# Kernel optimization log

Measured on AMD Instinct MI355X. Metric: run time of the kernel, lower is better.

Reference implementation:

```python
import jax, jax.numpy as jnp
import numpy as np

N, M, D, E, NLAYER = 200000, 100000, 64, 1000000, 3
EPS = 0.1
TLEN = (24, 7)


def l2norm(x):
    # F.normalize(dim=-1) with eps=1e-12 clamp on the norm
    n = jnp.linalg.norm(x, axis=-1, keepdims=True)
    return x / jnp.maximum(n, 1e-12)


def setup_inputs() -> dict:
    key = jax.random.key(0)
    ks = jax.random.split(key, 8)
    u_id = jax.random.randint(ks[0], (E,), 0, N)
    i_id = jax.random.randint(ks[1], (E,), 0, M)
    T = jnp.stack([
        jax.random.randint(ks[2], (E,), 0, TLEN[0]),
        jax.random.randint(ks[3], (E,), 0, TLEN[1]),
    ], axis=1)
    # xavier-uniform-ish init for embedding tables
    lim_u = np.sqrt(6.0 / (N + D)).astype(np.float32)
    lim_i = np.sqrt(6.0 / (M + D)).astype(np.float32)
    user_emb = jax.random.uniform(ks[4], (N, D), minval=-lim_u, maxval=lim_u)
    item_emb = jax.random.uniform(ks[5], (M, D), minval=-lim_i, maxval=lim_i)
    # xavier-normal time tables, each [tlen_i, D//tdim]
    W0 = jax.random.normal(ks[6], (TLEN[0], D // 2)) * np.sqrt(2.0 / (TLEN[0] + D // 2))
    W1 = jax.random.normal(ks[7], (TLEN[1], D // 2)) * np.sqrt(2.0 / (TLEN[1] + D // 2))
    beta = jnp.float32(0.3)
    return {"u_id": u_id, "i_id": i_id, "T": T, "beta": beta,
            "user_emb": user_emb, "item_emb": item_emb, "W0": W0, "W1": W1}


def _forward(u_id, i_id, T, beta, user_emb, item_emb, W0, W1):
    # TimeEncoder: one_hot(t) @ W == W[t]; concat over time dims -> [E, D]
    t_emb = jnp.concatenate([W0[T[:, 0]], W1[T[:, 1]]], axis=-1)
    u_t = l2norm(user_emb[u_id] + t_emb)
    i_t = l2norm(item_emb[i_id] + t_emb)
    s = ((u_t * i_t).sum(axis=-1) + 1.0) * 0.5      # cosine sim mapped to [0,1]
    s = jnp.where(s < beta, 0.0, s)                  # threshold

    # coalesced sparse COO mm: duplicates are summed by segment_sum anyway
    def spmm_u(X):  # A_r @ X : [n, d]
        return jax.ops.segment_sum(s[:, None] * X[i_id], u_id, num_segments=N)

    def spmm_i(X):  # A_r.T @ X : [m, d]
        return jax.ops.segment_sum(s[:, None] * X[u_id], i_id, num_segments=M)

    # pass 1: clean propagation
    u_embs, i_embs = [user_emb], [item_emb]
    for _ in range(NLAYER):
        u_embs.append(spmm_u(i_embs[-1]))
        i_embs.append(spmm_i(u_embs[-2]))
    u_fwd = jnp.mean(jnp.stack(u_embs[1:], 0), 0)
    i_fwd = jnp.mean(jnp.stack(i_embs[1:], 0), 0)

    # passes 2 & 3: perturbed propagation with randperm-row noise
    def perturbed_pass(base_key):
        u_embs, i_embs = [user_emb], [item_emb]
        for l in range(NLAYER):
            ku, ki = jax.random.split(jax.random.fold_in(base_key, l))
            u_emb = spmm_u(i_embs[-1])
            i_emb = spmm_i(u_embs[-1])
            u_emb = u_emb + l2norm(u_emb[jax.random.permutation(ku, N)]) * EPS
            i_emb = i_emb + l2norm(i_emb[jax.random.permutation(ki, M)]) * EPS
            u_embs.append(u_emb)
            i_embs.append(i_emb)
        return (jnp.mean(jnp.stack(u_embs[1:], 0), 0),
                jnp.mean(jnp.stack(i_embs[1:], 0), 0))

    u_p1, i_p1 = perturbed_pass(jax.random.key(1))
    u_p2, i_p2 = perturbed_pass(jax.random.key(2))
    return u_fwd, i_fwd, u_p1, i_p1, u_p2, i_p2


def reference(u_id, i_id, T, beta, user_emb, item_emb, W0, W1):
    return _forward(u_id, i_id, T, beta, user_emb, item_emb, W0, W1)
```

## Files before the change

### kernel.cpp

```cpp
#include <hip/hip_runtime.h>
#include <stdint.h>

#define NU 200000
#define NI 100000
#define DD 64
#define NE 1000000
#define EPSV 0.1f
#define NBUCK 65536
#define NSORT 12
#define PAIR (NU + NI)
#define TOTSORT (6 * PAIR)
#define NBALL (NSORT * NBUCK)
#define SCAN_TPB 256
#define SCAN_ELEMS 1024
#define CEILDIV(a,b) (((a)+(b)-1)/(b))

__host__ __device__ inline void tf2x32(uint32_t k0, uint32_t k1,
                                       uint32_t x0, uint32_t x1,
                                       uint32_t &o0, uint32_t &o1) {
  uint32_t ks0 = k0, ks1 = k1, ks2 = k0 ^ k1 ^ 0x1BD11BDAu;
  x0 += ks0; x1 += ks1;
#define TF_RND(r) { x0 += x1; x1 = (x1 << (r)) | (x1 >> (32 - (r))); x1 ^= x0; }
  TF_RND(13) TF_RND(15) TF_RND(26) TF_RND(6)   x0 += ks1; x1 += ks2 + 1u;
  TF_RND(17) TF_RND(29) TF_RND(16) TF_RND(24)  x0 += ks2; x1 += ks0 + 2u;
  TF_RND(13) TF_RND(15) TF_RND(26) TF_RND(6)   x0 += ks0; x1 += ks1 + 3u;
  TF_RND(17) TF_RND(29) TF_RND(16) TF_RND(24)  x0 += ks1; x1 += ks2 + 4u;
  TF_RND(13) TF_RND(15) TF_RND(26) TF_RND(6)   x0 += ks2; x1 += ks0 + 5u;
#undef TF_RND
  o0 = x0; o1 = x1;
}

struct K2 { uint32_t a, b; };
static inline K2 h_tf(K2 k, uint32_t x0, uint32_t x1) {
  K2 r; tf2x32(k.a, k.b, x0, x1, r.a, r.b); return r;
}

struct SortKeys { uint32_t a[NSORT]; uint32_t b[NSORT]; };

__device__ inline void regionOf(int gid, int &r, int &local) {
  int pairIdx = gid / PAIR;
  int rem = gid - pairIdx * PAIR;
  if (rem < NU) { r = pairIdx * 2;     local = rem; }
  else          { r = pairIdx * 2 + 1; local = rem - NU; }
}

__global__ void k_edge(const int* __restrict__ u_id, const int* __restrict__ i_id,
                       const int* __restrict__ T, const float* __restrict__ betap,
                       const float* __restrict__ UE, const float* __restrict__ IE,
                       const float* __restrict__ W0, const float* __restrict__ W1,
                       float* __restrict__ s)
{
  int g = blockIdx.x * blockDim.x + threadIdx.x;
  int e = g >> 4, lane = g & 15;
  if (e >= NE) return;
  int u = u_id[e], it = i_id[e];
  float4 a = ((const float4*)UE)[u * 16 + lane];
  float4 b = ((const float4*)IE)[it * 16 + lane];
  float4 t;
  if (lane < 8) t = ((const float4*)W0)[T[2 * e] * 8 + lane];
  else          t = ((const float4*)W1)[T[2 * e + 1] * 8 + (lane - 8)];
  float ux = a.x + t.x, uy = a.y + t.y, uz = a.z + t.z, uw = a.w + t.w;
  float ix = b.x + t.x, iy = b.y + t.y, iz = b.z + t.z, iw = b.w + t.w;
  float uu = ux * ux + uy * uy + uz * uz + uw * uw;
  float ii = ix * ix + iy * iy + iz * iz + iw * iw;
  float ui = ux * ix + uy * iy + uz * iz + uw * iw;
#pragma unroll
  for (int m = 1; m < 16; m <<= 1) {
    uu += __shfl_xor(uu, m);
    ii += __shfl_xor(ii, m);
    ui += __shfl_xor(ui, m);
  }
  if (lane == 0) {
    float c = ui / (fmaxf(sqrtf(uu), 1e-12f) * fmaxf(sqrtf(ii), 1e-12f));
    float sv = (c + 1.0f) * 0.5f;
    s[e] = (sv < betap[0]) ? 0.0f : sv;
  }
}

__global__ void k_scan1(const int* __restrict__ in, int n, int* __restrict__ partials)
{
  __shared__ int sdata[SCAN_TPB];
  int base = blockIdx.x * SCAN_ELEMS;
  int sum = 0;
  for (int j = threadIdx.x; j < SCAN_ELEMS; j += SCAN_TPB) {
    int idx = base + j;
    if (idx < n) sum += in[idx];
  }
  sdata[threadIdx.x] = sum;
  __syncthreads();
  for (int off = SCAN_TPB / 2; off > 0; off >>= 1) {
    if (threadIdx.x < off) sdata[threadIdx.x] += sdata[threadIdx.x + off];
    __syncthreads();
  }
  if (threadIdx.x == 0) partials[blockIdx.x] = sdata[0];
}

__global__ void k_scan2(int* __restrict__ partials, int nb, int* __restrict__ endPtr)
{
  __shared__ int part[1024];
  int tid = threadIdx.x;
  part[tid] = (tid < nb) ? partials[tid] : 0;
  __syncthreads();
  for (int off = 1; off < 1024; off <<= 1) {
    int t = (tid >= off) ? part[tid - off] : 0;
    __syncthreads();
    part[tid] += t;
    __syncthreads();
  }
  if (tid < nb) partials[tid] = tid ? part[tid - 1] : 0;
  if (tid == 1023 && endPtr) *endPtr = part[1023];
}

__global__ void k_scan3(const int* __restrict__ in, int n,
                        const int* __restrict__ partials,
                        int* __restrict__ offs, int* __restrict__ cursor)
{
  __shared__ int sdata[SCAN_TPB];
  int base = blockIdx.x * SCAN_ELEMS + threadIdx.x * 4;
  int v[4];
#pragma unroll
  for (int q = 0; q < 4; ++q) v[q] = (base + q < n) ? in[base + q] : 0;
  int tsum = v[0] + v[1] + v[2] + v[3];
  sdata[threadIdx.x] = tsum;
  __syncthreads();
  for (int off = 1; off < SCAN_TPB; off <<= 1) {
    int t = (threadIdx.x >= off) ? sdata[threadIdx.x - off] : 0;
    __syncthreads();
    sdata[threadIdx.x] += t;
    __syncthreads();
  }
  int excl = partials[blockIdx.x] + (threadIdx.x ? sdata[threadIdx.x - 1] : 0);
#pragma unroll
  for (int q = 0; q < 4; ++q) {
    if (base + q < n) {
      offs[base + q] = excl;
      if (cursor) cursor[base + q] = excl;
      excl += v[q];
    }
  }
}

static void scan_ex(hipStream_t st, const int* in, int n, int* offs, int* cursor,
                    int* partials, int* endPtr)
{
  int nb = CEILDIV(n, SCAN_ELEMS);
  k_scan1<<<nb, SCAN_TPB, 0, st>>>(in, n, partials);
  k_scan2<<<1, 1024, 0, st>>>(partials, nb, endPtr);
  k_scan3<<<nb, SCAN_TPB, 0, st>>>(in, n, partials, offs, cursor);
}

__global__ void k_count(const int* __restrict__ u_id, const int* __restrict__ i_id,
                        int* __restrict__ cnt_u, int* __restrict__ cnt_i)
{
  int e = blockIdx.x * blockDim.x + threadIdx.x;
  if (e < NE) {
    atomicAdd(&cnt_u[u_id[e]], 1);
    atomicAdd(&cnt_i[i_id[e]], 1);
  }
}

__global__ void k_scatter_csr(const int* __restrict__ u_id, const int* __restrict__ i_id,
                              const float* __restrict__ s,
                              int* __restrict__ cur_u, int* __restrict__ cur_i,
                              int* __restrict__ col_u, float* __restrict__ w_u,
                              int* __restrict__ col_i, float* __restrict__ w_i)
{
  int e = blockIdx.x * blockDim.x + threadIdx.x;
  if (e < NE) {
    float w = s[e];
    int pu = atomicAdd(&cur_u[u_id[e]], 1);
    col_u[pu] = i_id[e]; w_u[pu] = w;
    int pi = atomicAdd(&cur_i[i_id[e]], 1);
    col_i[pi] = u_id[e]; w_i[pi] = w;
  }
}

__global__ void k_spmm(const int* __restrict__ ptr, const int* __restrict__ col,
                       const float* __restrict__ w, const float* __restrict__ X,
                       float* __restrict__ Y, float* __restrict__ acc,
                       int nrows, int first, float scale)
{
  int g = blockIdx.x * blockDim.x + threadIdx.x;
  int r = g >> 4, lane = g & 15;
  if (r >= nrows) return;
  int b = ptr[r], e2 = ptr[r + 1];
  float4 a = make_float4(0.f, 0.f, 0.f, 0.f);
  for (int k = b; k < e2; ++k) {
    float wk = w[k];
    int c = col[k];
    float4 x = ((const float4*)X)[c * 16 + lane];
    a.x += wk * x.x; a.y += wk * x.y; a.z += wk * x.z; a.w += wk * x.w;
  }
  ((float4*)Y)[r * 16 + lane] = a;
  if (acc) {
    float4 v;
    if (first) v = a;
    else {
      v = ((const float4*)acc)[r * 16 + lane];
      v.x += a.x; v.y += a.y; v.z += a.z; v.w += a.w;
    }
    v.x *= scale; v.y *= scale; v.z *= scale; v.w *= scale;
    ((float4*)acc)[r * 16 + lane] = v;
  }
}

__global__ void k_noise(const float* __restrict__ S, const int* __restrict__ perm,
                        float* __restrict__ O, float* __restrict__ acc,
                        int nrows, int first, float scale)
{
  int g = blockIdx.x * blockDim.x + threadIdx.x;
  int r = g >> 4, lane = g & 15;
  if (r >= nrows) return;
  int pr = perm[r];
  float4 z = ((const float4*)S)[pr * 16 + lane];
  float ss = z.x * z.x + z.y * z.y + z.z * z.z + z.w * z.w;
#pragma unroll
  for (int m = 1; m < 16; m <<= 1) ss += __shfl_xor(ss, m);
  float coef = EPSV / fmaxf(sqrtf(ss), 1e-12f);
  float4 v = ((const float4*)S)[r * 16 + lane];
  v.x += coef * z.x; v.y += coef * z.y; v.z += coef * z.z; v.w += coef * z.w;
  ((float4*)O)[r * 16 + lane] = v;
  float4 a;
  if (first) a = v;
  else {
    a = ((const float4*)acc)[r * 16 + lane];
    a.x += v.x; a.y += v.y; a.z += v.z; a.w += v.w;
  }
  a.x *= scale; a.y *= scale; a.z *= scale; a.w *= scale;
  ((float4*)acc)[r * 16 + lane] = a;
}

__global__ void k_genkeys_all(SortKeys sk, uint32_t* __restrict__ keys)
{
  int gid = blockIdx.x * blockDim.x + threadIdx.x;
  if (gid >= TOTSORT) return;
  int r, local; regionOf(gid, r, local);
  uint32_t o0, o1;
  tf2x32(sk.a[r], sk.b[r], 0u, (uint32_t)local, o0, o1);
  keys[gid] = o0 ^ o1;
}

__global__ void k_hist_all(const uint32_t* __restrict__ keys, int* __restrict__ hist)
{
  int gid = blockIdx.x * blockDim.x + threadIdx.x;
  if (gid >= TOTSORT) return;
  int r, local; regionOf(gid, r, local);
  atomicAdd(&hist[r * NBUCK + (keys[gid] >> 16)], 1);
}

__global__ void k_scatter_all(const uint32_t* __restrict__ keys,
                              const int* __restrict__ valsIn,
                              int* __restrict__ cursor,
                              uint32_t* __restrict__ keyO, int* __restrict__ valO,
                              int* __restrict__ posO)
{
  int gid = blockIdx.x * blockDim.x + threadIdx.x;
  if (gid >= TOTSORT) return;
  int r, local; regionOf(gid, r, local);
  uint32_t k = keys[gid];
  int p = atomicAdd(&cursor[r * NBUCK + (k >> 16)], 1);
  keyO[p] = k;
  valO[p] = valsIn ? valsIn[gid] : local;
  posO[p] = local;
}

__global__ void k_fixup(const int* __restrict__ offs, uint32_t* __restrict__ keyO,
                        int* __restrict__ valO, int* __restrict__ posO)
{
  int b = blockIdx.x * blockDim.x + threadIdx.x;
  if (b >= NBALL) return;
  int s0 = offs[b], e0 = offs[b + 1];
  for (int i = s0 + 1; i < e0; ++i) {
    uint32_t k = keyO[i]; int v = valO[i], p = posO[i];
    int j = i - 1;
    while (j >= s0 && (keyO[j] > k || (keyO[j] == k && posO[j] > p))) {
      keyO[j + 1] = keyO[j]; valO[j + 1] = valO[j]; posO[j + 1] = posO[j];
      --j;
    }
    keyO[j + 1] = k; valO[j + 1] = v; posO[j + 1] = p;
  }
}

extern "C" void kernel_launch(void* const* d_in, const int* in_sizes, int n_in,
                              void* d_out, int out_size, void* d_ws, size_t ws_size,
                              hipStream_t stream)
{
  const int*   u_id = (const int*)d_in[0];
  const int*   i_id = (const int*)d_in[1];
  const int*   T    = (const int*)d_in[2];
  const float* beta = (const float*)d_in[3];
  const float* UE   = (const float*)d_in[4];
  const float* IE   = (const float*)d_in[5];
  const float* W0   = (const float*)d_in[6];
  const float* W1   = (const float*)d_in[7];
  (void)in_sizes; (void)n_in; (void)out_size; (void)ws_size;

  float* out   = (float*)d_out;
  float* o_ufw = out;
  float* o_ifw = o_ufw + (size_t)NU * DD;
  float* o_up1 = o_ifw + (size_t)NI * DD;
  float* o_ip1 = o_up1 + (size_t)NU * DD;
  float* o_up2 = o_ip1 + (size_t)NI * DD;
  float* o_ip2 = o_up2 + (size_t)NU * DD;

  char* wp = (char*)d_ws;
  auto carve = [&](size_t bytes) -> char* {
    char* r = wp; wp += (bytes + 255) & ~(size_t)255; return r;
  };
  int*      ptr_u    = (int*)  carve(4ull * (NU + 1));
  int*      cnt_u    = (int*)  carve(4ull * NU);
  int*      cur_u    = (int*)  carve(4ull * NU);
  int*      ptr_i    = (int*)  carve(4ull * (NI + 1));
  int*      cnt_i    = (int*)  carve(4ull * NI);
  int*      cur_i    = (int*)  carve(4ull * NI);
  int*      col_u    = (int*)  carve(4ull * NE);
  float*    w_u      = (float*)carve(4ull * NE);
  int*      col_i    = (int*)  carve(4ull * NE);
  float*    w_i      = (float*)carve(4ull * NE);
  int*      perms    = (int*)  carve(4ull * TOTSORT);
  int*      partials = (int*)  carve(4ull * 1025);
  char*     uni      =         carve(4ull * 2 * (size_t)(NU + NI) * DD);

  float* U1 = (float*)uni;
  float* U2 = U1 + (size_t)NU * DD;
  float* I1 = U2 + (size_t)NU * DD;
  float* I2 = I1 + (size_t)NI * DD;
  float* s = (float*)uni;
  uint32_t* keysA = (uint32_t*)uni;
  uint32_t* keyB  = keysA + TOTSORT;
  int*      posB  = (int*)(keyB + TOTSORT);
  int*      val0  = posB + TOTSORT;
  int*      hist  = val0 + TOTSORT;
  int*      offs  = hist + NBALL;
  int*      curs  = offs + NBALL + 1;

  k_edge<<<CEILDIV(NE * 16, 256), 256, 0, stream>>>(u_id, i_id, T, beta, UE, IE, W0, W1, s);

  hipMemsetAsync(cnt_u, 0, 4 * NU, stream);
  hipMemsetAsync(cnt_i, 0, 4 * NI, stream);
  k_count<<<CEILDIV(NE, 256), 256, 0, stream>>>(u_id, i_id, cnt_u, cnt_i);
  scan_ex(stream, cnt_u, NU, ptr_u, cur_u, partials, &ptr_u[NU]);
  scan_ex(stream, cnt_i, NI, ptr_i, cur_i, partials, &ptr_i[NI]);
  k_scatter_csr<<<CEILDIV(NE, 256), 256, 0, stream>>>(u_id, i_id, s, cur_u, cur_i,
                                                      col_u, w_u, col_i, w_i);

  SortKeys sk0, sk1;
  for (int p = 0; p < 2; ++p) {
    K2 base = {0u, (uint32_t)(p + 1)};
    for (int l = 0; l < 3; ++l) {
      K2 kl = h_tf(base, 0u, (uint32_t)l);
      K2 kk[2] = { h_tf(kl, 0u, 0u), h_tf(kl, 0u, 1u) };
      for (int q = 0; q < 2; ++q) {
        int r = (p * 3 + l) * 2 + q;
        K2 kperm = kk[q];
        K2 knext = h_tf(kperm, 0u, 0u);
        K2 sub0  = h_tf(kperm, 0u, 1u);
        K2 sub1  = h_tf(knext, 0u, 1u);
        sk0.a[r] = sub0.a; sk0.b[r] = sub0.b;
        sk1.a[r] = sub1.a; sk1.b[r] = sub1.b;
      }
    }
  }
  const int GS = CEILDIV(TOTSORT, 256), GF = CEILDIV(NBALL, 256);
  k_genkeys_all<<<GS, 256, 0, stream>>>(sk0, keysA);
  hipMemsetAsync(hist, 0, 4ull * NBALL, stream);
  k_hist_all<<<GS, 256, 0, stream>>>(keysA, hist);
  scan_ex(stream, hist, NBALL, offs, curs, partials, &offs[NBALL]);
  k_scatter_all<<<GS, 256, 0, stream>>>(keysA, (const int*)nullptr, curs, keyB, val0, posB);
  k_fixup<<<GF, 256, 0, stream>>>(offs, keyB, val0, posB);
  k_genkeys_all<<<GS, 256, 0, stream>>>(sk1, keysA);
  hipMemsetAsync(hist, 0, 4ull * NBALL, stream);
  k_hist_all<<<GS, 256, 0, stream>>>(keysA, hist);
  scan_ex(stream, hist, NBALL, offs, curs, partials, &offs[NBALL]);
  k_scatter_all<<<GS, 256, 0, stream>>>(keysA, val0, curs, keyB, perms, posB);
  k_fixup<<<GF, 256, 0, stream>>>(offs, keyB, perms, posB);

  const int GU = CEILDIV(NU * 16, 256), GI = CEILDIV(NI * 16, 256);
  const float THIRD = 1.0f / 3.0f;

  k_spmm<<<GU, 256, 0, stream>>>(ptr_u, col_u, w_u, IE, U1, o_ufw, NU, 1, 1.0f);
  k_spmm<<<GI, 256, 0, stream>>>(ptr_i, col_i, w_i, UE, I1, o_ifw, NI, 1, 1.0f);
  k_spmm<<<GU, 256, 0, stream>>>(ptr_u, col_u, w_u, I1, U2, o_ufw, NU, 0, 1.0f);
  k_spmm<<<GI, 256, 0, stream>>>(ptr_i, col_i, w_i, U1, I2, o_ifw, NI, 0, 1.0f);
  k_spmm<<<GU, 256, 0, stream>>>(ptr_u, col_u, w_u, I2, U1, o_ufw, NU, 0, THIRD);
  k_spmm<<<GI, 256, 0, stream>>>(ptr_i, col_i, w_i, U2, I1, o_ifw, NI, 0, THIRD);

  for (int p = 0; p < 2; ++p) {
    float* accU = (p == 0) ? o_up1 : o_up2;
    float* accI = (p == 0) ? o_ip1 : o_ip2;
    const float* uP = UE;
    const float* iP = IE;
    for (int l = 0; l < 3; ++l) {
      int* permU = perms + (size_t)(p * 3 + l) * PAIR;
      int* permI = permU + NU;
      int first = (l == 0), isLast = (l == 2);
      float sc = isLast ? THIRD : 1.0f;
      k_spmm<<<GU, 256, 0, stream>>>(ptr_u, col_u, w_u, iP, U1, (float*)nullptr, NU, 0, 1.0f);
      k_spmm<<<GI, 256, 0, stream>>>(ptr_i, col_i, w_i, uP, I1, (float*)nullptr, NI, 0, 1.0f);
      k_noise<<<GU, 256, 0, stream>>>(U1, permU, U2, accU, NU, first, sc);
      k_noise<<<GI, 256, 0, stream>>>(I1, permI, I2, accI, NI, first, sc);
      uP = U2; iP = I2;
    }
  }
}
```

Baseline: 2.301 ms.

## Fuse edge scoring with CSR scatter, merge user/item SpMM, reuse first-layer propagation

Edge similarity is now computed and scattered straight into CSR, storing column index and weight together as one uint2. This removes the separate scatter kernel and the round trip through the s array. User and item SpMM and noise kernels now run as single launches over both row sets. When workspace allows a third buffer, the first-layer propagation of the clean pass is reused by both perturbed passes, since all three start from the same input embeddings. Unneeded intermediate writes are skipped on last layers, at the cost of more workspace and a branchy combined kernel.

New measurement: 1.957 ms. 15.0% less time.

```diff
diff --git a/kernel.cpp b/kernel.cpp
--- a/kernel.cpp
+++ b/kernel.cpp
@@ -44,11 +44,12 @@
   else          { r = pairIdx * 2 + 1; local = rem - NU; }
 }
 
-__global__ void k_edge(const int* __restrict__ u_id, const int* __restrict__ i_id,
-                       const int* __restrict__ T, const float* __restrict__ betap,
-                       const float* __restrict__ UE, const float* __restrict__ IE,
-                       const float* __restrict__ W0, const float* __restrict__ W1,
-                       float* __restrict__ s)
+__global__ void k_edgesc(const int* __restrict__ u_id, const int* __restrict__ i_id,
+                         const int* __restrict__ T, const float* __restrict__ betap,
+                         const float* __restrict__ UE, const float* __restrict__ IE,
+                         const float* __restrict__ W0, const float* __restrict__ W1,
+                         int* __restrict__ cur_u, int* __restrict__ cur_i,
+                         uint2* __restrict__ colw_u, uint2* __restrict__ colw_i)
 {
   int g = blockIdx.x * blockDim.x + threadIdx.x;
   int e = g >> 4, lane = g & 15;
@@ -73,7 +74,12 @@
   if (lane == 0) {
     float c = ui / (fmaxf(sqrtf(uu), 1e-12f) * fmaxf(sqrtf(ii), 1e-12f));
     float sv = (c + 1.0f) * 0.5f;
-    s[e] = (sv < betap[0]) ? 0.0f : sv;
+    float w = (sv < betap[0]) ? 0.0f : sv;
+    uint32_t wb = __float_as_uint(w);
+    int pu = atomicAdd(&cur_u[u], 1);
+    colw_u[pu] = make_uint2((uint32_t)it, wb);
+    int pi = atomicAdd(&cur_i[it], 1);
+    colw_i[pi] = make_uint2((uint32_t)u, wb);
   }
 }
 
@@ -159,39 +165,28 @@
   }
 }
 
-__global__ void k_scatter_csr(const int* __restrict__ u_id, const int* __restrict__ i_id,
-                              const float* __restrict__ s,
-                              int* __restrict__ cur_u, int* __restrict__ cur_i,
-                              int* __restrict__ col_u, float* __restrict__ w_u,
-                              int* __restrict__ col_i, float* __restrict__ w_i)
-{
-  int e = blockIdx.x * blockDim.x + threadIdx.x;
-  if (e < NE) {
-    float w = s[e];
-    int pu = atomicAdd(&cur_u[u_id[e]], 1);
-    col_u[pu] = i_id[e]; w_u[pu] = w;
-    int pi = atomicAdd(&cur_i[i_id[e]], 1);
-    col_i[pi] = u_id[e]; w_i[pi] = w;
-  }
-}
-
-__global__ void k_spmm(const int* __restrict__ ptr, const int* __restrict__ col,
-                       const float* __restrict__ w, const float* __restrict__ X,
-                       float* __restrict__ Y, float* __restrict__ acc,
-                       int nrows, int first, float scale)
+__global__ void k_spmm2(const int* __restrict__ ptr_u, const uint2* __restrict__ colw_u,
+                        const float* __restrict__ Xi_in,
+                        const int* __restrict__ ptr_i, const uint2* __restrict__ colw_i,
+                        const float* __restrict__ Xu_in,
+                        float* __restrict__ Y, float* __restrict__ acc,
+                        int first, float scale, int writeY)
 {
   int g = blockIdx.x * blockDim.x + threadIdx.x;
   int r = g >> 4, lane = g & 15;
-  if (r >= nrows) return;
-  int b = ptr[r], e2 = ptr[r + 1];
+  if (r >= PAIR) return;
+  const int* ptr; const uint2* colw; const float4* X; int rr;
+  if (r < NU) { ptr = ptr_u; colw = colw_u; X = (const float4*)Xi_in; rr = r; }
+  else        { ptr = ptr_i; colw = colw_i; X = (const float4*)Xu_in; rr = r - NU; }
+  int b = ptr[rr], e2 = ptr[rr + 1];
   float4 a = make_float4(0.f, 0.f, 0.f, 0.f);
   for (int k = b; k < e2; ++k) {
-    float wk = w[k];
-    int c = col[k];
-    float4 x = ((const float4*)X)[c * 16 + lane];
+    uint2 cw = colw[k];
+    float wk = __uint_as_float(cw.y);
+    float4 x = X[(size_t)cw.x * 16 + lane];
     a.x += wk * x.x; a.y += wk * x.y; a.z += wk * x.z; a.w += wk * x.w;
   }
-  ((float4*)Y)[r * 16 + lane] = a;
+  if (writeY) ((float4*)Y)[r * 16 + lane] = a;
   if (acc) {
     float4 v;
     if (first) v = a;
@@ -204,22 +199,22 @@
   }
 }
 
-__global__ void k_noise(const float* __restrict__ S, const int* __restrict__ perm,
-                        float* __restrict__ O, float* __restrict__ acc,
-                        int nrows, int first, float scale)
+__global__ void k_noise2(const float* __restrict__ S, const int* __restrict__ perm,
+                         float* __restrict__ O, float* __restrict__ acc,
+                         int first, float scale, int writeO)
 {
   int g = blockIdx.x * blockDim.x + threadIdx.x;
   int r = g >> 4, lane = g & 15;
-  if (r >= nrows) return;
-  int pr = perm[r];
-  float4 z = ((const float4*)S)[pr * 16 + lane];
+  if (r >= PAIR) return;
+  int pr = (r < NU) ? perm[r] : NU + perm[r];
+  float4 z = ((const float4*)S)[(size_t)pr * 16 + lane];
   float ss = z.x * z.x + z.y * z.y + z.z * z.z + z.w * z.w;
 #pragma unroll
   for (int m = 1; m < 16; m <<= 1) ss += __shfl_xor(ss, m);
   float coef = EPSV / fmaxf(sqrtf(ss), 1e-12f);
-  float4 v = ((const float4*)S)[r * 16 + lane];
+  float4 v = ((const float4*)S)[(size_t)r * 16 + lane];
   v.x += coef * z.x; v.y += coef * z.y; v.z += coef * z.z; v.w += coef * z.w;
-  ((float4*)O)[r * 16 + lane] = v;
+  if (writeO) ((float4*)O)[r * 16 + lane] = v;
   float4 a;
   if (first) a = v;
   else {
@@ -293,39 +288,37 @@
   const float* IE   = (const float*)d_in[5];
   const float* W0   = (const float*)d_in[6];
   const float* W1   = (const float*)d_in[7];
-  (void)in_sizes; (void)n_in; (void)out_size; (void)ws_size;
-
-  float* out   = (float*)d_out;
-  float* o_ufw = out;
-  float* o_ifw = o_ufw + (size_t)NU * DD;
-  float* o_up1 = o_ifw + (size_t)NI * DD;
-  float* o_ip1 = o_up1 + (size_t)NU * DD;
-  float* o_up2 = o_ip1 + (size_t)NI * DD;
-  float* o_ip2 = o_up2 + (size_t)NU * DD;
+  (void)in_sizes; (void)n_in; (void)out_size;
+
+  float* out    = (float*)d_out;
+  float* accCln = out;
+  float* accP0  = out + (size_t)PAIR * DD;
+  float* accP1  = out + 2ull * PAIR * DD;
 
   char* wp = (char*)d_ws;
   auto carve = [&](size_t bytes) -> char* {
     char* r = wp; wp += (bytes + 255) & ~(size_t)255; return r;
   };
-  int*      ptr_u    = (int*)  carve(4ull * (NU + 1));
-  int*      cnt_u    = (int*)  carve(4ull * NU);
-  int*      cur_u    = (int*)  carve(4ull * NU);
-  int*      ptr_i    = (int*)  carve(4ull * (NI + 1));
-  int*      cnt_i    = (int*)  carve(4ull * NI);
-  int*      cur_i    = (int*)  carve(4ull * NI);
-  int*      col_u    = (int*)  carve(4ull * NE);
-  float*    w_u      = (float*)carve(4ull * NE);
-  int*      col_i    = (int*)  carve(4ull * NE);
-  float*    w_i      = (float*)carve(4ull * NE);
-  int*      perms    = (int*)  carve(4ull * TOTSORT);
-  int*      partials = (int*)  carve(4ull * 1025);
-  char*     uni      =         carve(4ull * 2 * (size_t)(NU + NI) * DD);
-
-  float* U1 = (float*)uni;
-  float* U2 = U1 + (size_t)NU * DD;
-  float* I1 = U2 + (size_t)NU * DD;
-  float* I2 = I1 + (size_t)NI * DD;
-  float* s = (float*)uni;
+  int*   ptr_u    = (int*)  carve(4ull * (NU + 1));
+  int*   cnt_u    = (int*)  carve(4ull * NU);
+  int*   cur_u    = (int*)  carve(4ull * NU);
+  int*   ptr_i    = (int*)  carve(4ull * (NI + 1));
+  int*   cnt_i    = (int*)  carve(4ull * NI);
+  int*   cur_i    = (int*)  carve(4ull * NI);
+  uint2* colw_u   = (uint2*)carve(8ull * NE);
+  uint2* colw_i   = (uint2*)carve(8ull * NE);
+  int*   perms    = (int*)  carve(4ull * TOTSORT);
+  int*   partials = (int*)  carve(4ull * 1025);
+
+  const size_t PB = (size_t)PAIR * DD * 4;
+  size_t used = (size_t)(wp - (char*)d_ws);
+  bool share = ws_size >= used + 3 * PB;
+  char* uni = carve(share ? 3 * PB : 2 * PB);
+
+  float* P0 = (float*)uni;
+  float* P1 = P0 + (size_t)PAIR * DD;
+  float* P2 = share ? P1 + (size_t)PAIR * DD : nullptr;
+
   uint32_t* keysA = (uint32_t*)uni;
   uint32_t* keyB  = keysA + TOTSORT;
   int*      posB  = (int*)(keyB + TOTSORT);
@@ -334,15 +327,14 @@
   int*      offs  = hist + NBALL;
   int*      curs  = offs + NBALL + 1;
 
-  k_edge<<<CEILDIV(NE * 16, 256), 256, 0, stream>>>(u_id, i_id, T, beta, UE, IE, W0, W1, s);
-
   hipMemsetAsync(cnt_u, 0, 4 * NU, stream);
   hipMemsetAsync(cnt_i, 0, 4 * NI, stream);
   k_count<<<CEILDIV(NE, 256), 256, 0, stream>>>(u_id, i_id, cnt_u, cnt_i);
   scan_ex(stream, cnt_u, NU, ptr_u, cur_u, partials, &ptr_u[NU]);
   scan_ex(stream, cnt_i, NI, ptr_i, cur_i, partials, &ptr_i[NI]);
-  k_scatter_csr<<<CEILDIV(NE, 256), 256, 0, stream>>>(u_id, i_id, s, cur_u, cur_i,
-                                                      col_u, w_u, col_i, w_i);
+  k_edgesc<<<CEILDIV(NE * 16, 256), 256, 0, stream>>>(u_id, i_id, T, beta, UE, IE,
+                                                      W0, W1, cur_u, cur_i,
+                                                      colw_u, colw_i);
 
   SortKeys sk0, sk1;
   for (int p = 0; p < 2; ++p) {
@@ -375,31 +367,43 @@
   k_scatter_all<<<GS, 256, 0, stream>>>(keysA, val0, curs, keyB, perms, posB);
   k_fixup<<<GF, 256, 0, stream>>>(offs, keyB, perms, posB);
 
-  const int GU = CEILDIV(NU * 16, 256), GI = CEILDIV(NI * 16, 256);
+  const int GP = CEILDIV(PAIR * 16, 256);
   const float THIRD = 1.0f / 3.0f;
-
-  k_spmm<<<GU, 256, 0, stream>>>(ptr_u, col_u, w_u, IE, U1, o_ufw, NU, 1, 1.0f);
-  k_spmm<<<GI, 256, 0, stream>>>(ptr_i, col_i, w_i, UE, I1, o_ifw, NI, 1, 1.0f);
-  k_spmm<<<GU, 256, 0, stream>>>(ptr_u, col_u, w_u, I1, U2, o_ufw, NU, 0, 1.0f);
-  k_spmm<<<GI, 256, 0, stream>>>(ptr_i, col_i, w_i, U1, I2, o_ifw, NI, 0, 1.0f);
-  k_spmm<<<GU, 256, 0, stream>>>(ptr_u, col_u, w_u, I2, U1, o_ufw, NU, 0, THIRD);
-  k_spmm<<<GI, 256, 0, stream>>>(ptr_i, col_i, w_i, U2, I1, o_ifw, NI, 0, THIRD);
-
-  for (int p = 0; p < 2; ++p) {
-    float* accU = (p == 0) ? o_up1 : o_up2;
-    float* accI = (p == 0) ? o_ip1 : o_ip2;
-    const float* uP = UE;
-    const float* iP = IE;
-    for (int l = 0; l < 3; ++l) {
-      int* permU = perms + (size_t)(p * 3 + l) * PAIR;
-      int* permI = permU + NU;
-      int first = (l == 0), isLast = (l == 2);
-      float sc = isLast ? THIRD : 1.0f;
-      k_spmm<<<GU, 256, 0, stream>>>(ptr_u, col_u, w_u, iP, U1, (float*)nullptr, NU, 0, 1.0f);
-      k_spmm<<<GI, 256, 0, stream>>>(ptr_i, col_i, w_i, uP, I1, (float*)nullptr, NI, 0, 1.0f);
-      k_noise<<<GU, 256, 0, stream>>>(U1, permU, U2, accU, NU, first, sc);
-      k_noise<<<GI, 256, 0, stream>>>(I1, permI, I2, accI, NI, first, sc);
-      uP = U2; iP = I2;
-    }
-  }
-}
+  auto SPMM = [&](const float* Xi_in, const float* Xu_in, float* Y, float* acc,
+                  int first, float scale, int writeY) {
+    k_spmm2<<<GP, 256, 0, stream>>>(ptr_u, colw_u, Xi_in, ptr_i, colw_i, Xu_in,
+                                    Y, acc, first, scale, writeY);
+  };
+  auto NOISE = [&](const float* S, int pass, int layer, float* O, float* acc,
+                   int first, float scale, int writeO) {
+    k_noise2<<<GP, 256, 0, stream>>>(S, perms + (size_t)(pass * 3 + layer) * PAIR,
+                                     O, acc, first, scale, writeO);
+  };
+
+  if (share) {
+    SPMM(IE, UE, P0, accCln, 1, 1.0f, 1);
+    SPMM(P0 + (size_t)NU * DD, P0, P1, accCln, 0, 1.0f, 1);
+    SPMM(P1 + (size_t)NU * DD, P1, nullptr, accCln, 0, THIRD, 0);
+    for (int p = 0; p < 2; ++p) {
+      float* acc = p ? accP1 : accP0;
+      NOISE(P0, p, 0, P1, acc, 1, 1.0f, 1);
+      SPMM(P1 + (size_t)NU * DD, P1, P2, nullptr, 0, 1.0f, 1);
+      NOISE(P2, p, 1, P1, acc, 0, 1.0f, 1);
+      SPMM(P1 + (size_t)NU * DD, P1, P2, nullptr, 0, 1.0f, 1);
+      NOISE(P2, p, 2, nullptr, acc, 0, THIRD, 0);
+    }
+  } else {
+    SPMM(IE, UE, P0, accCln, 1, 1.0f, 1);
+    SPMM(P0 + (size_t)NU * DD, P0, P1, accCln, 0, 1.0f, 1);
+    SPMM(P1 + (size_t)NU * DD, P1, nullptr, accCln, 0, THIRD, 0);
+    for (int p = 0; p < 2; ++p) {
+      float* acc = p ? accP1 : accP0;
+      SPMM(IE, UE, P0, nullptr, 0, 1.0f, 1);
+      NOISE(P0, p, 0, P1, acc, 1, 1.0f, 1);
+      SPMM(P1 + (size_t)NU * DD, P1, P0, nullptr, 0, 1.0f, 1);
+      NOISE(P0, p, 1, P1, acc, 0, 1.0f, 1);
+      SPMM(P1 + (size_t)NU * DD, P1, P0, nullptr, 0, 1.0f, 1);
+      NOISE(P0, p, 2, nullptr, acc, 0, THIRD, 0);
+    }
+  }
+}
```
